# Optimization experiments

Hardware: AMD Instinct MI355X
Metric: run time of the kernel (lower is better)

## Reference

```python
import jax, jax.numpy as jnp
import numpy as np

N = 100000   # nodes (single node type)
E = 160000   # edges per relation
R = 4        # relations
D_IN = 128
D_OUT = 128


def setup_inputs() -> dict:
    key = jax.random.key(0)
    k_x, k_w, k_lw, k_s, k_d = jax.random.split(key, 5)
    x = jax.random.normal(k_x, (N, D_IN), dtype=jnp.float32)
    # xavier-ish scale for weights
    scale = np.float32(np.sqrt(2.0 / (D_IN + D_OUT)))
    W = jax.random.normal(k_w, (R, D_IN, D_OUT), dtype=jnp.float32) * scale
    loop_weight = jax.random.normal(k_lw, (D_IN, D_OUT), dtype=jnp.float32) * scale
    src = jax.random.randint(k_s, (R, E), 0, N, dtype=jnp.int64)
    dst = jax.random.randint(k_d, (R, E), 0, N, dtype=jnp.int64)
    return {"x": x, "W": W, "loop_weight": loop_weight, "src": src, "dst": dst}


def reference(x, W, loop_weight, src, dst):
    # Per-relation linear transform: [R, N, D_OUT]
    h = jnp.einsum('nd,rde->rne', x, W)

    def rel_aggregate(hr, s, d):
        # gather messages at src, sum into dst, normalize by dst in-degree ('right' norm)
        msg = hr[s]                                            # [E, D_OUT]
        agg = jax.ops.segment_sum(msg, d, num_segments=N)      # [N, D_OUT]
        deg = jax.ops.segment_sum(jnp.ones(s.shape, hr.dtype), d, num_segments=N)
        return agg / jnp.clip(deg, 1.0)[:, None]

    per_rel = jax.vmap(rel_aggregate)(h, src, dst)             # [R, N, D_OUT]
    out = per_rel.sum(axis=0) + x @ loop_weight                # sum over relations + self-loop
    return jax.nn.relu(out)                                    # activation; dropout=0 -> identity
```

## Files before the change

### kernel.cpp

```cpp
#include <hip/hip_runtime.h>

#define D 128
#define TN 64
#define NC 8
#define NCHK 2

typedef __attribute__((ext_vector_type(8))) short short8;
typedef __attribute__((ext_vector_type(4))) float f32x4;

__device__ __forceinline__ unsigned int bf16rne(float f) {
  unsigned int b = __float_as_uint(f);
  return (b + 0x7fffu + ((b >> 16) & 1u)) >> 16;
}
__device__ __forceinline__ float bf2f(unsigned int u) {
  return __uint_as_float(u << 16);
}

__global__ __launch_bounds__(256) void rgc_prep(
    const float* __restrict__ x, const float* __restrict__ W,
    const float* __restrict__ loopW, unsigned short* __restrict__ xb,
    unsigned short* __restrict__ WT, uint4* __restrict__ zbase,
    long long zb16, int R, long long total8, int xblocks, int wblocks)
{
  if ((int)blockIdx.x < xblocks) {
    long long i = (long long)blockIdx.x * 256 + threadIdx.x;
    if (i >= total8) return;
    float4 v0 = ((const float4*)x)[i * 2];
    float4 v1 = ((const float4*)x)[i * 2 + 1];
    uint4 u;
    u.x = bf16rne(v0.x) | (bf16rne(v0.y) << 16);
    u.y = bf16rne(v0.z) | (bf16rne(v0.w) << 16);
    u.z = bf16rne(v1.x) | (bf16rne(v1.y) << 16);
    u.w = bf16rne(v1.z) | (bf16rne(v1.w) << 16);
    ((uint4*)xb)[i] = u;
  } else if ((int)blockIdx.x < xblocks + wblocks) {
    int tid = (blockIdx.x - xblocks) * 256 + threadIdx.x;
    int s = tid >> 14;
    if (s > R) return;
    int rem = tid & 16383;
    int k = rem >> 7;
    int c = rem & 127;
    float v = (s < R) ? W[(size_t)s * D * D + k * D + c] : loopW[k * D + c];
    unsigned int u = bf16rne(v);
    unsigned int off = ((unsigned int)(c * D + k) * 2u) ^ (((unsigned int)(c & 7)) << 4);
    *(unsigned short*)((char*)WT + (size_t)s * D * D * 2 + off) = (unsigned short)u;
  } else {
    long long i = (long long)(blockIdx.x - xblocks - wblocks) * 256 + threadIdx.x;
    if (i < zb16) zbase[i] = make_uint4(0, 0, 0, 0);
  }
}

__global__ __launch_bounds__(256) void rgc_hist(
    const int* __restrict__ dst, int* __restrict__ cnt8, int N, int E, int R)
{
  int r = blockIdx.y;
  int e = blockIdx.x * 256 + threadIdx.x;
  if (e >= E) return;
  int k = (blockIdx.x + gridDim.x * blockIdx.y) & (NC - 1);
  int d = dst[(size_t)r * E + e];
  atomicAdd(&cnt8[((size_t)k * R + r) * N + d], 1);
}

__global__ __launch_bounds__(256) void rgc_offsets(
    const int* __restrict__ cnt8, int* __restrict__ rowctr8,
    int* __restrict__ off8, int* __restrict__ nodeptr, int* __restrict__ degv,
    int N, int E, int R, int nt256, int nchunks)
{
  __shared__ int wtot[4];
  __shared__ int wbase[4];
  __shared__ int sbase;

  int chunk = blockIdx.x;
  if (chunk >= nchunks) return;
  int kx = blockIdx.x & (NC - 1);
  int r = chunk / nt256, t = chunk - r * nt256;
  int tid = threadIdx.x;
  int wv = tid >> 6, lane = tid & 63;
  int node = t * 256 + tid;

  int ck[NC];
  int deg = 0;
  if (node < N) {
#pragma unroll
    for (int k = 0; k < NC; k++) {
      ck[k] = cnt8[((size_t)k * R + r) * N + node];
      deg += ck[k];
    }
  } else {
#pragma unroll
    for (int k = 0; k < NC; k++) ck[k] = 0;
  }
  int v = deg;
#pragma unroll
  for (int o = 1; o < 64; o <<= 1) {
    int tsh = __shfl_up(v, o, 64);
    if (lane >= o) v += tsh;
  }
  if (lane == 63) wtot[wv] = v;
  __syncthreads();
  if (tid == 0) {
    int run = 0;
#pragma unroll
    for (int i = 0; i < 4; i++) { wbase[i] = run; run += wtot[i]; }
    sbase = atomicAdd(&rowctr8[kx * R + r], run);
  }
  __syncthreads();

  if (node < N) {
    int start = (kx * R + r) * E + sbase + wbase[wv] + (v - deg);
    nodeptr[(size_t)r * N + node] = start;
    degv[(size_t)r * N + node] = deg;
    int run = start;
#pragma unroll
    for (int k = 0; k < NC; k++) {
      off8[((size_t)k * R + r) * N + node] = run;
      run += ck[k];
    }
  }
}

__global__ __launch_bounds__(256) void rgc_fill(
    const int* __restrict__ src, const int* __restrict__ dst,
    int* __restrict__ off8, int* __restrict__ esrc, int N, int E, int R)
{
  int r = blockIdx.y;
  int e = blockIdx.x * 256 + threadIdx.x;
  if (e >= E) return;
  int k = (blockIdx.x + gridDim.x * blockIdx.y) & (NC - 1);
  int d = dst[(size_t)r * E + e];
  int pos = atomicAdd(&off8[((size_t)k * R + r) * N + d], 1);
  esrc[pos] = src[(size_t)r * E + e];
}

__global__ __launch_bounds__(256) void rgc_agg(
    const unsigned short* __restrict__ xb, const int* __restrict__ nodeptr,
    const int* __restrict__ degv, const int* __restrict__ esrc,
    unsigned short* __restrict__ Ahat, int N, int R, int tile0)
{
  int tx = threadIdx.x;
  int ltile = blockIdx.x;
  int tile = tile0 + ltile;
  int r = blockIdx.y;
  int node0 = tile * TN;
  int grp = tx >> 4, c = tx & 15;
  char* dstp = (char*)(Ahat + ((size_t)ltile * R + r) * (TN * D));

#pragma unroll
  for (int t = 0; t < 4; t++) {
    int row = grp * 4 + t;
    int node = node0 + row;
    float a[8];
#pragma unroll
    for (int q = 0; q < 8; q++) a[q] = 0.f;
    int deg = 0;
    if (node < N) {
      int st = nodeptr[(size_t)r * N + node];
      deg = degv[(size_t)r * N + node];
      for (int j = 0; j < deg; j++) {
        int s = esrc[st + j];
        uint4 u = ((const uint4*)(xb + (size_t)s * D))[c];
        a[0] += bf2f(u.x & 0xffffu); a[1] += bf2f(u.x >> 16);
        a[2] += bf2f(u.y & 0xffffu); a[3] += bf2f(u.y >> 16);
        a[4] += bf2f(u.z & 0xffffu); a[5] += bf2f(u.z >> 16);
        a[6] += bf2f(u.w & 0xffffu); a[7] += bf2f(u.w >> 16);
      }
    }
    float sc = 1.0f / fmaxf((float)deg, 1.0f);
    uint4 o;
    o.x = bf16rne(a[0] * sc) | (bf16rne(a[1] * sc) << 16);
    o.y = bf16rne(a[2] * sc) | (bf16rne(a[3] * sc) << 16);
    o.z = bf16rne(a[4] * sc) | (bf16rne(a[5] * sc) << 16);
    o.w = bf16rne(a[6] * sc) | (bf16rne(a[7] * sc) << 16);
    unsigned int off =
        ((unsigned int)(row * 256 + c * 16)) ^ (((unsigned int)(row & 7)) << 4);
    *(uint4*)(dstp + off) = o;
  }
}

__global__ __launch_bounds__(256) void rgc_gemm(
    const unsigned short* __restrict__ xb, const unsigned short* __restrict__ WT,
    const unsigned short* __restrict__ Ahat, float* __restrict__ out,
    int N, int R, int tile0)
{
  __shared__ char Ab[TN * D * 2];
  __shared__ char Wb[D * D * 2];

  int tx = threadIdx.x;
  int ltile = blockIdx.x;
  int tile = tile0 + ltile;
  int node0 = tile * TN;
  int lane = tx & 63;
  int w = tx >> 6;

  f32x4 acc[8];
#pragma unroll
  for (int i = 0; i < 8; i++) acc[i] = (f32x4){0.f, 0.f, 0.f, 0.f};

  for (int s = 0; s <= R; s++) {
    bool is_loop = (s == R);
    if (!is_loop) {
      const float4* asrc = (const float4*)(Ahat + ((size_t)ltile * R + s) * (TN * D));
#pragma unroll
      for (int i = 0; i < 4; i++)
        ((float4*)Ab)[tx + i * 256] = asrc[tx + i * 256];
    } else {
#pragma unroll
      for (int it = 0; it < 4; it++) {
        int i = tx + it * 256;
        int row = i >> 4, c16 = i & 15;
        int node = node0 + row;
        uint4 u = make_uint4(0, 0, 0, 0);
        if (node < N) u = ((const uint4*)(xb + (size_t)node * D))[c16];
        unsigned int off =
            ((unsigned int)(row * 256 + c16 * 16)) ^ (((unsigned int)(row & 7)) << 4);
        *(uint4*)(Ab + off) = u;
      }
    }
    const float4* wsrc = (const float4*)(WT + (size_t)s * D * D);
#pragma unroll
    for (int i = 0; i < 8; i++)
      ((float4*)Wb)[tx + i * 256] = wsrc[tx + i * 256];
    __syncthreads();

    int rA = w * 16 + (lane & 15);
    unsigned int mA = (unsigned int)((rA & 7) << 4);
    unsigned int kof = (unsigned int)((lane >> 4) * 16);
    short8 afr[4];
#pragma unroll
    for (int kk = 0; kk < 4; kk++)
      afr[kk] = *(const short8*)(Ab + rA * 256 + (((unsigned int)(kk * 64) + kof) ^ mA));
#pragma unroll
    for (int ct = 0; ct < 8; ct++) {
      int rB = ct * 16 + (lane & 15);
      unsigned int mB = (unsigned int)((rB & 7) << 4);
#pragma unroll
      for (int kk = 0; kk < 4; kk++) {
        short8 b = *(const short8*)(Wb + rB * 256 + (((unsigned int)(kk * 64) + kof) ^ mB));
        acc[ct] = __builtin_amdgcn_mfma_f32_16x16x32_bf16(afr[kk], b, acc[ct], 0, 0, 0);
      }
    }
    __syncthreads();
  }

  int colb = lane & 15;
  int rowb = (lane >> 4) * 4;
#pragma unroll
  for (int ct = 0; ct < 8; ct++) {
#pragma unroll
    for (int j = 0; j < 4; j++) {
      int node = node0 + w * 16 + rowb + j;
      if (node < N)
        out[(size_t)node * D + ct * 16 + colb] = fmaxf(acc[ct][j], 0.f);
    }
  }
}

extern "C" void kernel_launch(void* const* d_in, const int* in_sizes, int n_in,
                              void* d_out, int out_size, void* d_ws, size_t ws_size,
                              hipStream_t stream)
{
  const float* x     = (const float*)d_in[0];
  const float* W     = (const float*)d_in[1];
  const float* loopW = (const float*)d_in[2];
  const int*   src   = (const int*)d_in[3];
  const int*   dst   = (const int*)d_in[4];
  float* out = (float*)d_out;

  int N = in_sizes[0] / D;
  int R = in_sizes[1] / (D * D);
  int E = in_sizes[3] / R;
  int ntiles = (N + TN - 1) / TN;
  int ctmax = (ntiles + NCHK - 1) / NCHK;

  size_t o_cnt8  = 0;
  size_t o_rowc  = o_cnt8 + (size_t)NC * R * N * 4;
  size_t o_off8  = (o_rowc + (size_t)NC * R * 4 + 15) & ~(size_t)15;
  size_t o_np    = (o_off8 + (size_t)NC * R * N * 4 + 15) & ~(size_t)15;
  size_t o_deg   = (o_np + (size_t)R * N * 4 + 15) & ~(size_t)15;
  size_t o_esrc  = (o_deg + (size_t)R * N * 4 + 15) & ~(size_t)15;
  size_t o_wt    = (o_esrc + (size_t)NC * R * E * 4 + 15) & ~(size_t)15;
  size_t o_xb    = (o_wt + (size_t)(R + 1) * D * D * 2 + 15) & ~(size_t)15;
  size_t o_ahat  = (o_xb + (size_t)N * D * 2 + 15) & ~(size_t)15;

  char* wsb = (char*)d_ws;
  int*  cnt8    = (int*)(wsb + o_cnt8);
  int*  rowctr8 = (int*)(wsb + o_rowc);
  int*  off8    = (int*)(wsb + o_off8);
  int*  nodeptr = (int*)(wsb + o_np);
  int*  degv    = (int*)(wsb + o_deg);
  int*  esrc    = (int*)(wsb + o_esrc);
  unsigned short* WT   = (unsigned short*)(wsb + o_wt);
  unsigned short* xb   = (unsigned short*)(wsb + o_xb);
  unsigned short* Ahat = (unsigned short*)(wsb + o_ahat);

  long long total8 = (long long)N * D / 8;
  int xblocks = (int)((total8 + 255) / 256);
  int wblocks = ((R + 1) * D * D + 255) / 256;
  long long zb16 = (long long)(o_off8 - o_cnt8) / 16;
  int zblocks = (int)((zb16 + 255) / 256);
  rgc_prep<<<xblocks + wblocks + zblocks, 256, 0, stream>>>(
      x, W, loopW, xb, WT, (uint4*)wsb, zb16, R, total8, xblocks, wblocks);

  dim3 egrid((E + 255) / 256, R);
  rgc_hist<<<egrid, 256, 0, stream>>>(dst, cnt8, N, E, R);
  int nt256 = (N + 255) / 256;
  int nchunks = R * nt256;
  rgc_offsets<<<nchunks, 256, 0, stream>>>(
      cnt8, rowctr8, off8, nodeptr, degv, N, E, R, nt256, nchunks);
  rgc_fill<<<egrid, 256, 0, stream>>>(src, dst, off8, esrc, N, E, R);

  for (int c = 0; c < NCHK; c++) {
    int tile0 = c * ctmax;
    int ct = (ntiles - tile0 < ctmax) ? (ntiles - tile0) : ctmax;
    if (ct <= 0) break;
    dim3 agrid(ct, R);
    rgc_agg<<<agrid, 256, 0, stream>>>(xb, nodeptr, degv, esrc, Ahat, N, R, tile0);
    rgc_gemm<<<ct, 256, 0, stream>>>(xb, WT, Ahat, out, N, R, tile0);
  }
}
```

Before: 196.4 us.

## Overlap chunk gemm with next chunk aggregation in a combined kernel

Replaces the serial agg/gemm sequence over two chunks with a combined launch. It runs the gemm for the first chunk alongside the aggregation for the second chunk, using double-buffered Ahat workspaces. The neighbor gather loop is also unrolled by two to keep more independent loads in flight. The combined kernel carries the gemm's shared-memory footprint for aggregation blocks too, which may cut their occupancy, and the second Ahat buffer needs more workspace.

```diff
diff --git a/kernel.cpp b/kernel.cpp
--- a/kernel.cpp
+++ b/kernel.cpp
@@ -3,7 +3,6 @@
 #define D 128
 #define TN 64
 #define NC 8
-#define NCHK 2
 
 typedef __attribute__((ext_vector_type(8))) short short8;
 typedef __attribute__((ext_vector_type(4))) float f32x4;
@@ -132,15 +131,12 @@
   esrc[pos] = src[(size_t)r * E + e];
 }
 
-__global__ __launch_bounds__(256) void rgc_agg(
+__device__ __forceinline__ void agg_body(
     const unsigned short* __restrict__ xb, const int* __restrict__ nodeptr,
     const int* __restrict__ degv, const int* __restrict__ esrc,
-    unsigned short* __restrict__ Ahat, int N, int R, int tile0)
-{
-  int tx = threadIdx.x;
-  int ltile = blockIdx.x;
-  int tile = tile0 + ltile;
-  int r = blockIdx.y;
+    unsigned short* __restrict__ Ahat, int N, int R,
+    int ltile, int r, int tile, int tx)
+{
   int node0 = tile * TN;
   int grp = tx >> 4, c = tx & 15;
   char* dstp = (char*)(Ahat + ((size_t)ltile * R + r) * (TN * D));
@@ -156,13 +152,28 @@
     if (node < N) {
       int st = nodeptr[(size_t)r * N + node];
       deg = degv[(size_t)r * N + node];
-      for (int j = 0; j < deg; j++) {
-        int s = esrc[st + j];
-        uint4 u = ((const uint4*)(xb + (size_t)s * D))[c];
-        a[0] += bf2f(u.x & 0xffffu); a[1] += bf2f(u.x >> 16);
-        a[2] += bf2f(u.y & 0xffffu); a[3] += bf2f(u.y >> 16);
-        a[4] += bf2f(u.z & 0xffffu); a[5] += bf2f(u.z >> 16);
-        a[6] += bf2f(u.w & 0xffffu); a[7] += bf2f(u.w >> 16);
+      int j = 0;
+      for (; j + 2 <= deg; j += 2) {
+        int s0 = esrc[st + j];
+        int s1 = esrc[st + j + 1];
+        uint4 u0 = ((const uint4*)(xb + (size_t)s0 * D))[c];
+        uint4 u1 = ((const uint4*)(xb + (size_t)s1 * D))[c];
+        a[0] += bf2f(u0.x & 0xffffu) + bf2f(u1.x & 0xffffu);
+        a[1] += bf2f(u0.x >> 16)     + bf2f(u1.x >> 16);
+        a[2] += bf2f(u0.y & 0xffffu) + bf2f(u1.y & 0xffffu);
+        a[3] += bf2f(u0.y >> 16)     + bf2f(u1.y >> 16);
+        a[4] += bf2f(u0.z & 0xffffu) + bf2f(u1.z & 0xffffu);
+        a[5] += bf2f(u0.z >> 16)     + bf2f(u1.z >> 16);
+        a[6] += bf2f(u0.w & 0xffffu) + bf2f(u1.w & 0xffffu);
+        a[7] += bf2f(u0.w >> 16)     + bf2f(u1.w >> 16);
+      }
+      if (j < deg) {
+        int s0 = esrc[st + j];
+        uint4 u0 = ((const uint4*)(xb + (size_t)s0 * D))[c];
+        a[0] += bf2f(u0.x & 0xffffu); a[1] += bf2f(u0.x >> 16);
+        a[2] += bf2f(u0.y & 0xffffu); a[3] += bf2f(u0.y >> 16);
+        a[4] += bf2f(u0.z & 0xffffu); a[5] += bf2f(u0.z >> 16);
+        a[6] += bf2f(u0.w & 0xffffu); a[7] += bf2f(u0.w >> 16);
       }
     }
     float sc = 1.0f / fmaxf((float)deg, 1.0f);
@@ -177,17 +188,14 @@
   }
 }
 
-__global__ __launch_bounds__(256) void rgc_gemm(
+__device__ __forceinline__ void gemm_body(
     const unsigned short* __restrict__ xb, const unsigned short* __restrict__ WT,
     const unsigned short* __restrict__ Ahat, float* __restrict__ out,
-    int N, int R, int tile0)
+    int N, int R, int ltile, int tile, int tx)
 {
   __shared__ char Ab[TN * D * 2];
   __shared__ char Wb[D * D * 2];
 
-  int tx = threadIdx.x;
-  int ltile = blockIdx.x;
-  int tile = tile0 + ltile;
   int node0 = tile * TN;
   int lane = tx & 63;
   int w = tx >> 6;
@@ -255,6 +263,42 @@
   }
 }
 
+__global__ __launch_bounds__(256) void rgc_agg(
+    const unsigned short* __restrict__ xb, const int* __restrict__ nodeptr,
+    const int* __restrict__ degv, const int* __restrict__ esrc,
+    unsigned short* __restrict__ Ahat, int N, int R, int tile0)
+{
+  agg_body(xb, nodeptr, degv, esrc, Ahat, N, R,
+           blockIdx.x, blockIdx.y, tile0 + blockIdx.x, threadIdx.x);
+}
+
+__global__ __launch_bounds__(256) void rgc_gemm(
+    const unsigned short* __restrict__ xb, const unsigned short* __restrict__ WT,
+    const unsigned short* __restrict__ Ahat, float* __restrict__ out,
+    int N, int R, int tile0)
+{
+  gemm_body(xb, WT, Ahat, out, N, R, blockIdx.x, tile0 + blockIdx.x, threadIdx.x);
+}
+
+__global__ __launch_bounds__(256) void rgc_combo(
+    const unsigned short* __restrict__ xb, const unsigned short* __restrict__ WT,
+    const unsigned short* __restrict__ AhatR, unsigned short* __restrict__ AhatW,
+    const int* __restrict__ nodeptr, const int* __restrict__ degv,
+    const int* __restrict__ esrc, float* __restrict__ out,
+    int N, int R, int ct_gemm, int tile0_gemm, int ct_agg, int tile0_agg)
+{
+  int s = blockIdx.x;
+  int t = blockIdx.y;
+  if (s == 0) {
+    if (t < ct_gemm)
+      gemm_body(xb, WT, AhatR, out, N, R, t, tile0_gemm + t, threadIdx.x);
+  } else {
+    if (t < ct_agg)
+      agg_body(xb, nodeptr, degv, esrc, AhatW, N, R, t, s - 1, tile0_agg + t,
+               threadIdx.x);
+  }
+}
+
 extern "C" void kernel_launch(void* const* d_in, const int* in_sizes, int n_in,
                               void* d_out, int out_size, void* d_ws, size_t ws_size,
                               hipStream_t stream)
@@ -270,7 +314,7 @@
   int R = in_sizes[1] / (D * D);
   int E = in_sizes[3] / R;
   int ntiles = (N + TN - 1) / TN;
-  int ctmax = (ntiles + NCHK - 1) / NCHK;
+  int ctmax = (ntiles + 1) / 2;
 
   size_t o_cnt8  = 0;
   size_t o_rowc  = o_cnt8 + (size_t)NC * R * N * 4;
@@ -289,9 +333,10 @@
   int*  nodeptr = (int*)(wsb + o_np);
   int*  degv    = (int*)(wsb + o_deg);
   int*  esrc    = (int*)(wsb + o_esrc);
-  unsigned short* WT   = (unsigned short*)(wsb + o_wt);
-  unsigned short* xb   = (unsigned short*)(wsb + o_xb);
-  unsigned short* Ahat = (unsigned short*)(wsb + o_ahat);
+  unsigned short* WT    = (unsigned short*)(wsb + o_wt);
+  unsigned short* xb    = (unsigned short*)(wsb + o_xb);
+  unsigned short* Ahat0 = (unsigned short*)(wsb + o_ahat);
+  unsigned short* Ahat1 = Ahat0 + (size_t)ctmax * R * TN * D;
 
   long long total8 = (long long)N * D / 8;
   int xblocks = (int)((total8 + 255) / 256);
@@ -309,12 +354,17 @@
       cnt8, rowctr8, off8, nodeptr, degv, N, E, R, nt256, nchunks);
   rgc_fill<<<egrid, 256, 0, stream>>>(src, dst, off8, esrc, N, E, R);
 
-  for (int c = 0; c < NCHK; c++) {
-    int tile0 = c * ctmax;
-    int ct = (ntiles - tile0 < ctmax) ? (ntiles - tile0) : ctmax;
-    if (ct <= 0) break;
-    dim3 agrid(ct, R);
-    rgc_agg<<<agrid, 256, 0, stream>>>(xb, nodeptr, degv, esrc, Ahat, N, R, tile0);
-    rgc_gemm<<<ct, 256, 0, stream>>>(xb, WT, Ahat, out, N, R, tile0);
-  }
-}
+  int ct0 = ntiles < ctmax ? ntiles : ctmax;
+  int ct1 = ntiles - ct0;
+
+  dim3 agrid0(ct0, R);
+  rgc_agg<<<agrid0, 256, 0, stream>>>(xb, nodeptr, degv, esrc, Ahat0, N, R, 0);
+  if (ct1 > 0) {
+    dim3 cgrid(R + 1, ct0 > ct1 ? ct0 : ct1);
+    rgc_combo<<<cgrid, 256, 0, stream>>>(xb, WT, Ahat0, Ahat1, nodeptr, degv, esrc,
+                                         out, N, R, ct0, 0, ct1, ct0);
+    rgc_gemm<<<ct1, 256, 0, stream>>>(xb, WT, Ahat1, out, N, R, ct0);
+  } else {
+    rgc_gemm<<<ct0, 256, 0, stream>>>(xb, WT, Ahat0, out, N, R, 0);
+  }
+}
```

New measurement: 198.0 us. No clear change (+0.8%).

## Pack node ptr/degree, unroll gather by two, remap GEMM warp tiling

Applied to the files above, without the earlier changes.

Node start pointer and degree are stored together as one int2, so the aggregation kernel issues a single load instead of two. The neighbour gather loop is unrolled by two so two row loads are in flight at once. The GEMM is reorganised so each warp owns two column tiles across all four row tiles: B fragments stay in registers and A fragments are reloaded per row tile, which changes the LDS read pattern. This raises register use for B fragments and may lower occupancy.

```diff
diff --git a/kernel.cpp b/kernel.cpp
--- a/kernel.cpp
+++ b/kernel.cpp
@@ -3,7 +3,6 @@
 #define D 128
 #define TN 64
 #define NC 8
-#define NCHK 2
 
 typedef __attribute__((ext_vector_type(8))) short short8;
 typedef __attribute__((ext_vector_type(4))) float f32x4;
@@ -63,7 +62,7 @@
 
 __global__ __launch_bounds__(256) void rgc_offsets(
     const int* __restrict__ cnt8, int* __restrict__ rowctr8,
-    int* __restrict__ off8, int* __restrict__ nodeptr, int* __restrict__ degv,
+    int* __restrict__ off8, int2* __restrict__ npd,
     int N, int E, int R, int nt256, int nchunks)
 {
   __shared__ int wtot[4];
@@ -108,8 +107,7 @@
 
   if (node < N) {
     int start = (kx * R + r) * E + sbase + wbase[wv] + (v - deg);
-    nodeptr[(size_t)r * N + node] = start;
-    degv[(size_t)r * N + node] = deg;
+    npd[(size_t)r * N + node] = make_int2(start, deg);
     int run = start;
 #pragma unroll
     for (int k = 0; k < NC; k++) {
@@ -133,9 +131,9 @@
 }
 
 __global__ __launch_bounds__(256) void rgc_agg(
-    const unsigned short* __restrict__ xb, const int* __restrict__ nodeptr,
-    const int* __restrict__ degv, const int* __restrict__ esrc,
-    unsigned short* __restrict__ Ahat, int N, int R, int tile0)
+    const unsigned short* __restrict__ xb, const int2* __restrict__ npd,
+    const int* __restrict__ esrc, unsigned short* __restrict__ Ahat,
+    int N, int R, int tile0)
 {
   int tx = threadIdx.x;
   int ltile = blockIdx.x;
@@ -154,15 +152,31 @@
     for (int q = 0; q < 8; q++) a[q] = 0.f;
     int deg = 0;
     if (node < N) {
-      int st = nodeptr[(size_t)r * N + node];
-      deg = degv[(size_t)r * N + node];
-      for (int j = 0; j < deg; j++) {
-        int s = esrc[st + j];
-        uint4 u = ((const uint4*)(xb + (size_t)s * D))[c];
-        a[0] += bf2f(u.x & 0xffffu); a[1] += bf2f(u.x >> 16);
-        a[2] += bf2f(u.y & 0xffffu); a[3] += bf2f(u.y >> 16);
-        a[4] += bf2f(u.z & 0xffffu); a[5] += bf2f(u.z >> 16);
-        a[6] += bf2f(u.w & 0xffffu); a[7] += bf2f(u.w >> 16);
+      int2 sd = npd[(size_t)r * N + node];
+      int st = sd.x;
+      deg = sd.y;
+      int j = 0;
+      for (; j + 2 <= deg; j += 2) {
+        int s0 = esrc[st + j];
+        int s1 = esrc[st + j + 1];
+        uint4 u0 = ((const uint4*)(xb + (size_t)s0 * D))[c];
+        uint4 u1 = ((const uint4*)(xb + (size_t)s1 * D))[c];
+        a[0] += bf2f(u0.x & 0xffffu) + bf2f(u1.x & 0xffffu);
+        a[1] += bf2f(u0.x >> 16)     + bf2f(u1.x >> 16);
+        a[2] += bf2f(u0.y & 0xffffu) + bf2f(u1.y & 0xffffu);
+        a[3] += bf2f(u0.y >> 16)     + bf2f(u1.y >> 16);
+        a[4] += bf2f(u0.z & 0xffffu) + bf2f(u1.z & 0xffffu);
+        a[5] += bf2f(u0.z >> 16)     + bf2f(u1.z >> 16);
+        a[6] += bf2f(u0.w & 0xffffu) + bf2f(u1.w & 0xffffu);
+        a[7] += bf2f(u0.w >> 16)     + bf2f(u1.w >> 16);
+      }
+      if (j < deg) {
+        int s0 = esrc[st + j];
+        uint4 u0 = ((const uint4*)(xb + (size_t)s0 * D))[c];
+        a[0] += bf2f(u0.x & 0xffffu); a[1] += bf2f(u0.x >> 16);
+        a[2] += bf2f(u0.y & 0xffffu); a[3] += bf2f(u0.y >> 16);
+        a[4] += bf2f(u0.z & 0xffffu); a[5] += bf2f(u0.z >> 16);
+        a[6] += bf2f(u0.w & 0xffffu); a[7] += bf2f(u0.w >> 16);
       }
     }
     float sc = 1.0f / fmaxf((float)deg, 1.0f);
@@ -192,9 +206,13 @@
   int lane = tx & 63;
   int w = tx >> 6;
 
-  f32x4 acc[8];
-#pragma unroll
-  for (int i = 0; i < 8; i++) acc[i] = (f32x4){0.f, 0.f, 0.f, 0.f};
+  f32x4 acc[4][2];
+#pragma unroll
+  for (int i = 0; i < 4; i++)
+#pragma unroll
+    for (int j = 0; j < 2; j++) acc[i][j] = (f32x4){0.f, 0.f, 0.f, 0.f};
+
+  unsigned int kof = (unsigned int)((lane >> 4) * 16);
 
   for (int s = 0; s <= R; s++) {
     bool is_loop = (s == R);
@@ -222,22 +240,31 @@
       ((float4*)Wb)[tx + i * 256] = wsrc[tx + i * 256];
     __syncthreads();
 
-    int rA = w * 16 + (lane & 15);
-    unsigned int mA = (unsigned int)((rA & 7) << 4);
-    unsigned int kof = (unsigned int)((lane >> 4) * 16);
-    short8 afr[4];
-#pragma unroll
-    for (int kk = 0; kk < 4; kk++)
-      afr[kk] = *(const short8*)(Ab + rA * 256 + (((unsigned int)(kk * 64) + kof) ^ mA));
-#pragma unroll
-    for (int ct = 0; ct < 8; ct++) {
-      int rB = ct * 16 + (lane & 15);
+    short8 bfr[2][4];
+#pragma unroll
+    for (int ctl = 0; ctl < 2; ctl++) {
+      int rB = (2 * w + ctl) * 16 + (lane & 15);
       unsigned int mB = (unsigned int)((rB & 7) << 4);
 #pragma unroll
-      for (int kk = 0; kk < 4; kk++) {
-        short8 b = *(const short8*)(Wb + rB * 256 + (((unsigned int)(kk * 64) + kof) ^ mB));
-        acc[ct] = __builtin_amdgcn_mfma_f32_16x16x32_bf16(afr[kk], b, acc[ct], 0, 0, 0);
-      }
+      for (int kk = 0; kk < 4; kk++)
+        bfr[ctl][kk] =
+            *(const short8*)(Wb + rB * 256 + (((unsigned int)(kk * 64) + kof) ^ mB));
+    }
+#pragma unroll
+    for (int rt = 0; rt < 4; rt++) {
+      int rA = rt * 16 + (lane & 15);
+      unsigned int mA = (unsigned int)((rA & 7) << 4);
+      short8 afr[4];
+#pragma unroll
+      for (int kk = 0; kk < 4; kk++)
+        afr[kk] =
+            *(const short8*)(Ab + rA * 256 + (((unsigned int)(kk * 64) + kof) ^ mA));
+#pragma unroll
+      for (int ctl = 0; ctl < 2; ctl++)
+#pragma unroll
+        for (int kk = 0; kk < 4; kk++)
+          acc[rt][ctl] = __builtin_amdgcn_mfma_f32_16x16x32_bf16(
+              afr[kk], bfr[ctl][kk], acc[rt][ctl], 0, 0, 0);
     }
     __syncthreads();
   }
@@ -245,12 +272,16 @@
   int colb = lane & 15;
   int rowb = (lane >> 4) * 4;
 #pragma unroll
-  for (int ct = 0; ct < 8; ct++) {
-#pragma unroll
-    for (int j = 0; j < 4; j++) {
-      int node = node0 + w * 16 + rowb + j;
-      if (node < N)
-        out[(size_t)node * D + ct * 16 + colb] = fmaxf(acc[ct][j], 0.f);
+  for (int rt = 0; rt < 4; rt++) {
+#pragma unroll
+    for (int ctl = 0; ctl < 2; ctl++) {
+      int ct = 2 * w + ctl;
+#pragma unroll
+      for (int j = 0; j < 4; j++) {
+        int node = node0 + rt * 16 + rowb + j;
+        if (node < N)
+          out[(size_t)node * D + ct * 16 + colb] = fmaxf(acc[rt][ctl][j], 0.f);
+      }
     }
   }
 }
@@ -270,14 +301,13 @@
   int R = in_sizes[1] / (D * D);
   int E = in_sizes[3] / R;
   int ntiles = (N + TN - 1) / TN;
-  int ctmax = (ntiles + NCHK - 1) / NCHK;
+  int ctmax = (ntiles + 1) / 2;
 
   size_t o_cnt8  = 0;
   size_t o_rowc  = o_cnt8 + (size_t)NC * R * N * 4;
   size_t o_off8  = (o_rowc + (size_t)NC * R * 4 + 15) & ~(size_t)15;
-  size_t o_np    = (o_off8 + (size_t)NC * R * N * 4 + 15) & ~(size_t)15;
-  size_t o_deg   = (o_np + (size_t)R * N * 4 + 15) & ~(size_t)15;
-  size_t o_esrc  = (o_deg + (size_t)R * N * 4 + 15) & ~(size_t)15;
+  size_t o_npd   = (o_off8 + (size_t)NC * R * N * 4 + 15) & ~(size_t)15;
+  size_t o_esrc  = (o_npd + (size_t)R * N * 8 + 15) & ~(size_t)15;
   size_t o_wt    = (o_esrc + (size_t)NC * R * E * 4 + 15) & ~(size_t)15;
   size_t o_xb    = (o_wt + (size_t)(R + 1) * D * D * 2 + 15) & ~(size_t)15;
   size_t o_ahat  = (o_xb + (size_t)N * D * 2 + 15) & ~(size_t)15;
@@ -286,8 +316,7 @@
   int*  cnt8    = (int*)(wsb + o_cnt8);
   int*  rowctr8 = (int*)(wsb + o_rowc);
   int*  off8    = (int*)(wsb + o_off8);
-  int*  nodeptr = (int*)(wsb + o_np);
-  int*  degv    = (int*)(wsb + o_deg);
+  int2* npd     = (int2*)(wsb + o_npd);
   int*  esrc    = (int*)(wsb + o_esrc);
   unsigned short* WT   = (unsigned short*)(wsb + o_wt);
   unsigned short* xb   = (unsigned short*)(wsb + o_xb);
@@ -306,15 +335,15 @@
   int nt256 = (N + 255) / 256;
   int nchunks = R * nt256;
   rgc_offsets<<<nchunks, 256, 0, stream>>>(
-      cnt8, rowctr8, off8, nodeptr, degv, N, E, R, nt256, nchunks);
+      cnt8, rowctr8, off8, npd, N, E, R, nt256, nchunks);
   rgc_fill<<<egrid, 256, 0, stream>>>(src, dst, off8, esrc, N, E, R);
 
-  for (int c = 0; c < NCHK; c++) {
+  for (int c = 0; c < 2; c++) {
     int tile0 = c * ctmax;
     int ct = (ntiles - tile0 < ctmax) ? (ntiles - tile0) : ctmax;
     if (ct <= 0) break;
     dim3 agrid(ct, R);
-    rgc_agg<<<agrid, 256, 0, stream>>>(xb, nodeptr, degv, esrc, Ahat, N, R, tile0);
+    rgc_agg<<<agrid, 256, 0, stream>>>(xb, npd, esrc, Ahat, N, R, tile0);
     rgc_gemm<<<ct, 256, 0, stream>>>(xb, WT, Ahat, out, N, R, tile0);
   }
 }
```

Measured after the change: 184.8 us. -5.9%, faster.
